# Performance work log

Measured on AMD Instinct MI355X. Metric: run time of the kernel, lower is better.

Reference implementation:

```python
import jax, jax.numpy as jnp
import numpy as np

N_NODES = 100000
FEAT = 256      # input_size == out_size (required for multi-layer consistency in original code)
OUT = 256
B = 20000       # batch of target nodes
S = 25          # sampled neighbors per node (padded)


def setup_inputs() -> dict:
    key = jax.random.key(0)
    k1, k2, k3, k4, k5, k6 = jax.random.split(key, 6)
    feats = jax.random.normal(k1, (N_NODES, FEAT), dtype=jnp.float32)
    nodes = jax.random.randint(k2, (B,), 0, N_NODES)
    samp_neighs = jax.random.randint(k3, (B, S), 0, N_NODES)
    val_lens = jax.random.randint(k4, (B,), 1, S + 1)  # at least 1 valid neighbor
    # xavier_uniform-like scale for [out, 2*in] weights
    s0 = (6.0 / (OUT + 2 * FEAT)) ** 0.5
    s1 = (6.0 / (OUT + 2 * OUT)) ** 0.5
    w0 = jax.random.uniform(k5, (OUT, 2 * FEAT), jnp.float32, -s0, s0)
    w1 = jax.random.uniform(k6, (OUT, 2 * OUT), jnp.float32, -s1, s1)
    return {"feats": feats, "nodes": nodes, "samp_neighs": samp_neighs,
            "val_lens": val_lens, "w0": w0, "w1": w1}


def _mean_agg(neigh_feats, val_lens):
    # neigh_feats: [B, S, F]; ragged MEAN over first val_lens[b] neighbors
    mask = (jnp.arange(neigh_feats.shape[1])[None, :] < val_lens[:, None]).astype(neigh_feats.dtype)
    summed = jnp.einsum('bsf,bs->bf', neigh_feats, mask)
    return summed / val_lens[:, None].astype(neigh_feats.dtype)


def reference(feats, nodes, samp_neighs, val_lens, w0, w1):
    self_raw = feats[nodes]           # [B, F] gather
    neigh = feats[samp_neighs]        # [B, S, F] gather
    agg = _mean_agg(neigh, val_lens)  # [B, F]
    feat_data = self_raw
    for w in (w0, w1):
        # SageLayer: relu(W @ concat(self, agg).T).T == relu(concat @ W.T)
        combined = jnp.concatenate([self_raw, agg], axis=1)  # [B, 2F]
        feat_data = jax.nn.relu(combined @ w.T)              # [B, OUT]
        # Original recomputes aggregator with feat_data as self_feats, but MEAN
        # aggregation (gcn=False) depends only on raw neighbor feats -> identical.
        agg = _mean_agg(neigh, val_lens)
    return feat_data
```

## Files before the change

kernel.cpp:

```cpp
#include <hip/hip_runtime.h>

typedef unsigned short u16;
typedef unsigned int   u32;

#define NB     20000
#define SNB    25
#define FEAT   256
#define K2     512
#define OUTF   256

#define BM     16
#define NPW    4
#define LDA    520
#define BK     32
#define LDB    40
#define NCHUNK (K2 / BK)

typedef __attribute__((ext_vector_type(8))) short short8;
typedef __attribute__((ext_vector_type(4))) float f32x4;

__device__ __forceinline__ u32 f2bf(float f) {
  union { u32 i; float f; } x; x.f = f;
  return (x.i + 0x7fffu + ((x.i >> 16) & 1u)) >> 16;
}
__device__ __forceinline__ u32 pack2(float a, float b) {
  return f2bf(a) | (f2bf(b) << 16);
}

__global__ __launch_bounds__(256) void convw_kernel(
    const float* __restrict__ w_raw, u16* __restrict__ w_bf) {
  const int i = blockIdx.x * 256 + threadIdx.x;
  w_bf[i] = (u16)f2bf(w_raw[i]);
}

__global__ __launch_bounds__(256) void fused_kernel(
    const float* __restrict__ feats, const int* __restrict__ nodes,
    const int* __restrict__ neighs, const int* __restrict__ lens,
    const u16* __restrict__ W, float* __restrict__ C) {
  __shared__ u16 As[BM * LDA];
  __shared__ u16 Bs[OUTF * LDB];

  const int tid   = threadIdx.x;
  const int wave  = tid >> 6;
  const int lane  = tid & 63;
  const int mbase = blockIdx.x * BM;

  {
    const uint4* src = (const uint4*)(W + (size_t)tid * K2);
    uint4* dst = (uint4*)&Bs[tid * LDB];
#pragma unroll
    for (int c = 0; c < 4; ++c) dst[c] = src[c];
  }

  for (int p = 0; p < NPW; ++p) {
    const int m = wave * NPW + p;
    const int b = mbase + m;
    const int self = nodes[b];
    const int len  = lens[b];
    int myidx = (lane < SNB) ? neighs[b * SNB + lane] : 0;

    const float4 sv = ((const float4*)(feats + (size_t)self * FEAT))[lane];

    float4 a0 = {0.f, 0.f, 0.f, 0.f}, a1 = a0, a2 = a0, a3 = a0;
    float4 a4 = a0, a5 = a0, a6 = a0, a7 = a0;
    int s = 0;
    for (; s + 8 <= len; s += 8) {
      const int i0 = __shfl(myidx, s);
      const int i1 = __shfl(myidx, s + 1);
      const int i2 = __shfl(myidx, s + 2);
      const int i3 = __shfl(myidx, s + 3);
      const int i4 = __shfl(myidx, s + 4);
      const int i5 = __shfl(myidx, s + 5);
      const int i6 = __shfl(myidx, s + 6);
      const int i7 = __shfl(myidx, s + 7);
      const float4 v0 = ((const float4*)(feats + (size_t)i0 * FEAT))[lane];
      const float4 v1 = ((const float4*)(feats + (size_t)i1 * FEAT))[lane];
      const float4 v2 = ((const float4*)(feats + (size_t)i2 * FEAT))[lane];
      const float4 v3 = ((const float4*)(feats + (size_t)i3 * FEAT))[lane];
      const float4 v4 = ((const float4*)(feats + (size_t)i4 * FEAT))[lane];
      const float4 v5 = ((const float4*)(feats + (size_t)i5 * FEAT))[lane];
      const float4 v6 = ((const float4*)(feats + (size_t)i6 * FEAT))[lane];
      const float4 v7 = ((const float4*)(feats + (size_t)i7 * FEAT))[lane];
      a0.x += v0.x; a0.y += v0.y; a0.z += v0.z; a0.w += v0.w;
      a1.x += v1.x; a1.y += v1.y; a1.z += v1.z; a1.w += v1.w;
      a2.x += v2.x; a2.y += v2.y; a2.z += v2.z; a2.w += v2.w;
      a3.x += v3.x; a3.y += v3.y; a3.z += v3.z; a3.w += v3.w;
      a4.x += v4.x; a4.y += v4.y; a4.z += v4.z; a4.w += v4.w;
      a5.x += v5.x; a5.y += v5.y; a5.z += v5.z; a5.w += v5.w;
      a6.x += v6.x; a6.y += v6.y; a6.z += v6.z; a6.w += v6.w;
      a7.x += v7.x; a7.y += v7.y; a7.z += v7.z; a7.w += v7.w;
    }
    for (; s + 4 <= len; s += 4) {
      const int i0 = __shfl(myidx, s);
      const int i1 = __shfl(myidx, s + 1);
      const int i2 = __shfl(myidx, s + 2);
      const int i3 = __shfl(myidx, s + 3);
      const float4 v0 = ((const float4*)(feats + (size_t)i0 * FEAT))[lane];
      const float4 v1 = ((const float4*)(feats + (size_t)i1 * FEAT))[lane];
      const float4 v2 = ((const float4*)(feats + (size_t)i2 * FEAT))[lane];
      const float4 v3 = ((const float4*)(feats + (size_t)i3 * FEAT))[lane];
      a0.x += v0.x; a0.y += v0.y; a0.z += v0.z; a0.w += v0.w;
      a1.x += v1.x; a1.y += v1.y; a1.z += v1.z; a1.w += v1.w;
      a2.x += v2.x; a2.y += v2.y; a2.z += v2.z; a2.w += v2.w;
      a3.x += v3.x; a3.y += v3.y; a3.z += v3.z; a3.w += v3.w;
    }
    for (; s < len; ++s) {
      const int i0 = __shfl(myidx, s);
      const float4 v0 = ((const float4*)(feats + (size_t)i0 * FEAT))[lane];
      a0.x += v0.x; a0.y += v0.y; a0.z += v0.z; a0.w += v0.w;
    }
    a0.x += a4.x; a0.y += a4.y; a0.z += a4.z; a0.w += a4.w;
    a1.x += a5.x; a1.y += a5.y; a1.z += a5.z; a1.w += a5.w;
    a2.x += a6.x; a2.y += a6.y; a2.z += a6.z; a2.w += a6.w;
    a3.x += a7.x; a3.y += a7.y; a3.z += a7.z; a3.w += a7.w;
    const float inv = 1.f / (float)len;
    const float m0 = (a0.x + a1.x + a2.x + a3.x) * inv;
    const float m1 = (a0.y + a1.y + a2.y + a3.y) * inv;
    const float m2 = (a0.z + a1.z + a2.z + a3.z) * inv;
    const float m3 = (a0.w + a1.w + a2.w + a3.w) * inv;

    uint2* arow = (uint2*)&As[m * LDA];
    uint2 pe; pe.x = pack2(sv.x, sv.y); pe.y = pack2(sv.z, sv.w);
    arow[lane] = pe;
    uint2 pm; pm.x = pack2(m0, m1); pm.y = pack2(m2, m3);
    arow[64 + lane] = pm;
  }
  __syncthreads();

  const int wc  = wave * 64;
  const int r16 = lane & 15;
  const int kq  = (lane >> 4) * 8;

  f32x4 acc[4] = {};

  for (int kc = 0; ; ) {
    const int k0 = kc * BK;
    const short8 af = *(const short8*)&As[(r16)*LDA + k0 + kq];
    short8 bf[4];
#pragma unroll
    for (int j = 0; j < 4; ++j)
      bf[j] = *(const short8*)&Bs[(wc + j * 16 + r16) * LDB + kq];

#pragma unroll
    for (int j = 0; j < 4; ++j)
      acc[j] = __builtin_amdgcn_mfma_f32_16x16x32_bf16(af, bf[j], acc[j],
                                                       0, 0, 0);
    if (++kc == NCHUNK) break;
    __syncthreads();
    {
      const uint4* src = (const uint4*)(W + (size_t)tid * K2 + kc * BK);
      uint4* dst = (uint4*)&Bs[tid * LDB];
#pragma unroll
      for (int c = 0; c < 4; ++c) dst[c] = src[c];
    }
    __syncthreads();
  }

#pragma unroll
  for (int r = 0; r < 4; ++r) {
    const int row = mbase + (lane >> 4) * 4 + r;
#pragma unroll
    for (int j = 0; j < 4; ++j) {
      const int col = wc + j * 16 + r16;
      const float v = acc[j][r];
      C[(size_t)row * OUTF + col] = v > 0.f ? v : 0.f;
    }
  }
}

extern "C" void kernel_launch(void* const* d_in, const int* in_sizes, int n_in,
                              void* d_out, int out_size, void* d_ws, size_t ws_size,
                              hipStream_t stream) {
  const float* feats = (const float*)d_in[0];
  const int* nodes   = (const int*)d_in[1];
  const int* neighs  = (const int*)d_in[2];
  const int* lens    = (const int*)d_in[3];
  const float* w1    = (const float*)d_in[5];
  float* out = (float*)d_out;

  u16* w1bf = (u16*)d_ws;

  convw_kernel<<<512, 256, 0, stream>>>(w1, w1bf);
  fused_kernel<<<NB / BM, 256, 0, stream>>>(feats, nodes, neighs, lens, w1bf, out);
}
```

Before: 234.5 us.

## Split fused gather-GEMM kernel into separate aggregation and GEMM kernels

Splits the fused kernel into an aggregation kernel, which writes the bf16 concatenated [self, mean] rows to a workspace buffer, and a GEMM kernel that reads A and W straight from global memory with no LDS staging or barriers. The aim is to remove the many __syncthreads and LDS copies of W in the GEMM loop and to let the gather run at higher occupancy. The cost is an extra round trip of about 20 MB through global memory plus one more kernel launch, and the GEMM now depends on cache hits for its repeated W reads.

```diff
diff --git a/kernel.cpp b/kernel.cpp
--- a/kernel.cpp
+++ b/kernel.cpp
@@ -9,12 +9,7 @@
 #define K2     512
 #define OUTF   256
 
-#define BM     16
-#define NPW    4
-#define LDA    520
-#define BK     32
-#define LDB    40
-#define NCHUNK (K2 / BK)
+#define WS_W1_OFF (NB * K2 * 2)
 
 typedef __attribute__((ext_vector_type(8))) short short8;
 typedef __attribute__((ext_vector_type(4))) float f32x4;
@@ -33,127 +28,114 @@
   w_bf[i] = (u16)f2bf(w_raw[i]);
 }
 
-__global__ __launch_bounds__(256) void fused_kernel(
+__global__ __launch_bounds__(256) void agg_kernel(
     const float* __restrict__ feats, const int* __restrict__ nodes,
     const int* __restrict__ neighs, const int* __restrict__ lens,
-    const u16* __restrict__ W, float* __restrict__ C) {
-  __shared__ u16 As[BM * LDA];
-  __shared__ u16 Bs[OUTF * LDB];
+    u16* __restrict__ combined) {
+  const int b    = blockIdx.x * 4 + (threadIdx.x >> 6);
+  const int lane = threadIdx.x & 63;
 
+  const int self = nodes[b];
+  const int len  = lens[b];
+  int myidx = (lane < SNB) ? neighs[b * SNB + lane] : 0;
+
+  const float4 sv = ((const float4*)(feats + (size_t)self * FEAT))[lane];
+
+  float4 a0 = {0.f, 0.f, 0.f, 0.f}, a1 = a0, a2 = a0, a3 = a0;
+  float4 a4 = a0, a5 = a0, a6 = a0, a7 = a0;
+  int s = 0;
+  for (; s + 8 <= len; s += 8) {
+    const int i0 = __shfl(myidx, s);
+    const int i1 = __shfl(myidx, s + 1);
+    const int i2 = __shfl(myidx, s + 2);
+    const int i3 = __shfl(myidx, s + 3);
+    const int i4 = __shfl(myidx, s + 4);
+    const int i5 = __shfl(myidx, s + 5);
+    const int i6 = __shfl(myidx, s + 6);
+    const int i7 = __shfl(myidx, s + 7);
+    const float4 v0 = ((const float4*)(feats + (size_t)i0 * FEAT))[lane];
+    const float4 v1 = ((const float4*)(feats + (size_t)i1 * FEAT))[lane];
+    const float4 v2 = ((const float4*)(feats + (size_t)i2 * FEAT))[lane];
+    const float4 v3 = ((const float4*)(feats + (size_t)i3 * FEAT))[lane];
+    const float4 v4 = ((const float4*)(feats + (size_t)i4 * FEAT))[lane];
+    const float4 v5 = ((const float4*)(feats + (size_t)i5 * FEAT))[lane];
+    const float4 v6 = ((const float4*)(feats + (size_t)i6 * FEAT))[lane];
+    const float4 v7 = ((const float4*)(feats + (size_t)i7 * FEAT))[lane];
+    a0.x += v0.x; a0.y += v0.y; a0.z += v0.z; a0.w += v0.w;
+    a1.x += v1.x; a1.y += v1.y; a1.z += v1.z; a1.w += v1.w;
+    a2.x += v2.x; a2.y += v2.y; a2.z += v2.z; a2.w += v2.w;
+    a3.x += v3.x; a3.y += v3.y; a3.z += v3.z; a3.w += v3.w;
+    a4.x += v4.x; a4.y += v4.y; a4.z += v4.z; a4.w += v4.w;
+    a5.x += v5.x; a5.y += v5.y; a5.z += v5.z; a5.w += v5.w;
+    a6.x += v6.x; a6.y += v6.y; a6.z += v6.z; a6.w += v6.w;
+    a7.x += v7.x; a7.y += v7.y; a7.z += v7.z; a7.w += v7.w;
+  }
+  for (; s + 4 <= len; s += 4) {
+    const int i0 = __shfl(myidx, s);
+    const int i1 = __shfl(myidx, s + 1);
+    const int i2 = __shfl(myidx, s + 2);
+    const int i3 = __shfl(myidx, s + 3);
+    const float4 v0 = ((const float4*)(feats + (size_t)i0 * FEAT))[lane];
+    const float4 v1 = ((const float4*)(feats + (size_t)i1 * FEAT))[lane];
+    const float4 v2 = ((const float4*)(feats + (size_t)i2 * FEAT))[lane];
+    const float4 v3 = ((const float4*)(feats + (size_t)i3 * FEAT))[lane];
+    a0.x += v0.x; a0.y += v0.y; a0.z += v0.z; a0.w += v0.w;
+    a1.x += v1.x; a1.y += v1.y; a1.z += v1.z; a1.w += v1.w;
+    a2.x += v2.x; a2.y += v2.y; a2.z += v2.z; a2.w += v2.w;
+    a3.x += v3.x; a3.y += v3.y; a3.z += v3.z; a3.w += v3.w;
+  }
+  for (; s < len; ++s) {
+    const int i0 = __shfl(myidx, s);
+    const float4 v0 = ((const float4*)(feats + (size_t)i0 * FEAT))[lane];
+    a0.x += v0.x; a0.y += v0.y; a0.z += v0.z; a0.w += v0.w;
+  }
+  a0.x += a4.x; a0.y += a4.y; a0.z += a4.z; a0.w += a4.w;
+  a1.x += a5.x; a1.y += a5.y; a1.z += a5.z; a1.w += a5.w;
+  a2.x += a6.x; a2.y += a6.y; a2.z += a6.z; a2.w += a6.w;
+  a3.x += a7.x; a3.y += a7.y; a3.z += a7.z; a3.w += a7.w;
+  const float inv = 1.f / (float)len;
+  const float m0 = (a0.x + a1.x + a2.x + a3.x) * inv;
+  const float m1 = (a0.y + a1.y + a2.y + a3.y) * inv;
+  const float m2 = (a0.z + a1.z + a2.z + a3.z) * inv;
+  const float m3 = (a0.w + a1.w + a2.w + a3.w) * inv;
+
+  uint2* crow = (uint2*)(combined + (size_t)b * K2);
+  uint2 pe; pe.x = pack2(sv.x, sv.y); pe.y = pack2(sv.z, sv.w);
+  crow[lane] = pe;
+  uint2 pm; pm.x = pack2(m0, m1); pm.y = pack2(m2, m3);
+  crow[64 + lane] = pm;
+}
+
+__global__ __launch_bounds__(256) void gemm_kernel(
+    const u16* __restrict__ A,
+    const u16* __restrict__ W,
+    float* __restrict__ C) {
   const int tid   = threadIdx.x;
   const int wave  = tid >> 6;
   const int lane  = tid & 63;
-  const int mbase = blockIdx.x * BM;
-
-  {
-    const uint4* src = (const uint4*)(W + (size_t)tid * K2);
-    uint4* dst = (uint4*)&Bs[tid * LDB];
-#pragma unroll
-    for (int c = 0; c < 4; ++c) dst[c] = src[c];
-  }
-
-  for (int p = 0; p < NPW; ++p) {
-    const int m = wave * NPW + p;
-    const int b = mbase + m;
-    const int self = nodes[b];
-    const int len  = lens[b];
-    int myidx = (lane < SNB) ? neighs[b * SNB + lane] : 0;
-
-    const float4 sv = ((const float4*)(feats + (size_t)self * FEAT))[lane];
-
-    float4 a0 = {0.f, 0.f, 0.f, 0.f}, a1 = a0, a2 = a0, a3 = a0;
-    float4 a4 = a0, a5 = a0, a6 = a0, a7 = a0;
-    int s = 0;
-    for (; s + 8 <= len; s += 8) {
-      const int i0 = __shfl(myidx, s);
-      const int i1 = __shfl(myidx, s + 1);
-      const int i2 = __shfl(myidx, s + 2);
-      const int i3 = __shfl(myidx, s + 3);
-      const int i4 = __shfl(myidx, s + 4);
-      const int i5 = __shfl(myidx, s + 5);
-      const int i6 = __shfl(myidx, s + 6);
-      const int i7 = __shfl(myidx, s + 7);
-      const float4 v0 = ((const float4*)(feats + (size_t)i0 * FEAT))[lane];
-      const float4 v1 = ((const float4*)(feats + (size_t)i1 * FEAT))[lane];
-      const float4 v2 = ((const float4*)(feats + (size_t)i2 * FEAT))[lane];
-      const float4 v3 = ((const float4*)(feats + (size_t)i3 * FEAT))[lane];
-      const float4 v4 = ((const float4*)(feats + (size_t)i4 * FEAT))[lane];
-      const float4 v5 = ((const float4*)(feats + (size_t)i5 * FEAT))[lane];
-      const float4 v6 = ((const float4*)(feats + (size_t)i6 * FEAT))[lane];
-      const float4 v7 = ((const float4*)(feats + (size_t)i7 * FEAT))[lane];
-      a0.x += v0.x; a0.y += v0.y; a0.z += v0.z; a0.w += v0.w;
-      a1.x += v1.x; a1.y += v1.y; a1.z += v1.z; a1.w += v1.w;
-      a2.x += v2.x; a2.y += v2.y; a2.z += v2.z; a2.w += v2.w;
-      a3.x += v3.x; a3.y += v3.y; a3.z += v3.z; a3.w += v3.w;
-      a4.x += v4.x; a4.y += v4.y; a4.z += v4.z; a4.w += v4.w;
-      a5.x += v5.x; a5.y += v5.y; a5.z += v5.z; a5.w += v5.w;
-      a6.x += v6.x; a6.y += v6.y; a6.z += v6.z; a6.w += v6.w;
-      a7.x += v7.x; a7.y += v7.y; a7.z += v7.z; a7.w += v7.w;
-    }
-    for (; s + 4 <= len; s += 4) {
-      const int i0 = __shfl(myidx, s);
-      const int i1 = __shfl(myidx, s + 1);
-      const int i2 = __shfl(myidx, s + 2);
-      const int i3 = __shfl(myidx, s + 3);
-      const float4 v0 = ((const float4*)(feats + (size_t)i0 * FEAT))[lane];
-      const float4 v1 = ((const float4*)(feats + (size_t)i1 * FEAT))[lane];
-      const float4 v2 = ((const float4*)(feats + (size_t)i2 * FEAT))[lane];
-      const float4 v3 = ((const float4*)(feats + (size_t)i3 * FEAT))[lane];
-      a0.x += v0.x; a0.y += v0.y; a0.z += v0.z; a0.w += v0.w;
-      a1.x += v1.x; a1.y += v1.y; a1.z += v1.z; a1.w += v1.w;
-      a2.x += v2.x; a2.y += v2.y; a2.z += v2.z; a2.w += v2.w;
-      a3.x += v3.x; a3.y += v3.y; a3.z += v3.z; a3.w += v3.w;
-    }
-    for (; s < len; ++s) {
-      const int i0 = __shfl(myidx, s);
-      const float4 v0 = ((const float4*)(feats + (size_t)i0 * FEAT))[lane];
-      a0.x += v0.x; a0.y += v0.y; a0.z += v0.z; a0.w += v0.w;
-    }
-    a0.x += a4.x; a0.y += a4.y; a0.z += a4.z; a0.w += a4.w;
-    a1.x += a5.x; a1.y += a5.y; a1.z += a5.z; a1.w += a5.w;
-    a2.x += a6.x; a2.y += a6.y; a2.z += a6.z; a2.w += a6.w;
-    a3.x += a7.x; a3.y += a7.y; a3.z += a7.z; a3.w += a7.w;
-    const float inv = 1.f / (float)len;
-    const float m0 = (a0.x + a1.x + a2.x + a3.x) * inv;
-    const float m1 = (a0.y + a1.y + a2.y + a3.y) * inv;
-    const float m2 = (a0.z + a1.z + a2.z + a3.z) * inv;
-    const float m3 = (a0.w + a1.w + a2.w + a3.w) * inv;
-
-    uint2* arow = (uint2*)&As[m * LDA];
-    uint2 pe; pe.x = pack2(sv.x, sv.y); pe.y = pack2(sv.z, sv.w);
-    arow[lane] = pe;
-    uint2 pm; pm.x = pack2(m0, m1); pm.y = pack2(m2, m3);
-    arow[64 + lane] = pm;
-  }
-  __syncthreads();
+  const int mbase = blockIdx.x * 16;
 
   const int wc  = wave * 64;
   const int r16 = lane & 15;
   const int kq  = (lane >> 4) * 8;
 
+  const u16* arow = A + (size_t)(mbase + r16) * K2 + kq;
+  const u16* wrow = W + (size_t)(wc + r16) * K2 + kq;
+
   f32x4 acc[4] = {};
 
-  for (int kc = 0; ; ) {
-    const int k0 = kc * BK;
-    const short8 af = *(const short8*)&As[(r16)*LDA + k0 + kq];
+#pragma unroll 4
+  for (int kc = 0; kc < 16; ++kc) {
+    const int k0 = kc * 32;
+    const short8 af = *(const short8*)(arow + k0);
     short8 bf[4];
 #pragma unroll
     for (int j = 0; j < 4; ++j)
-      bf[j] = *(const short8*)&Bs[(wc + j * 16 + r16) * LDB + kq];
-
+      bf[j] = *(const short8*)(wrow + (size_t)j * 16 * K2 + k0);
 #pragma unroll
     for (int j = 0; j < 4; ++j)
       acc[j] = __builtin_amdgcn_mfma_f32_16x16x32_bf16(af, bf[j], acc[j],
                                                        0, 0, 0);
-    if (++kc == NCHUNK) break;
-    __syncthreads();
-    {
-      const uint4* src = (const uint4*)(W + (size_t)tid * K2 + kc * BK);
-      uint4* dst = (uint4*)&Bs[tid * LDB];
-#pragma unroll
-      for (int c = 0; c < 4; ++c) dst[c] = src[c];
-    }
-    __syncthreads();
   }
 
 #pragma unroll
@@ -178,8 +160,11 @@
   const float* w1    = (const float*)d_in[5];
   float* out = (float*)d_out;
 
-  u16* w1bf = (u16*)d_ws;
+  char* ws = (char*)d_ws;
+  u16* combined = (u16*)ws;
+  u16* w1bf     = (u16*)(ws + WS_W1_OFF);
 
   convw_kernel<<<512, 256, 0, stream>>>(w1, w1bf);
-  fused_kernel<<<NB / BM, 256, 0, stream>>>(feats, nodes, neighs, lens, w1bf, out);
+  agg_kernel<<<NB / 4, 256, 0, stream>>>(feats, nodes, neighs, lens, combined);
+  gemm_kernel<<<NB / 16, 256, 0, stream>>>(combined, w1bf, out);
 }
```

Result: faster. 228.1 us (-2.7%).
